# Kernel tuning notes

Hardware: AMD Instinct MI355X
Metric: run time of the kernel (lower is better)

Reference implementation:

```python
import jax, jax.numpy as jnp
import numpy as np

N, KLEN, Q, S, E, H = 8, 512, 16, 128, 256, 8


def setup_inputs() -> dict:
    key = jax.random.key(0)
    ks = jax.random.split(key, 9)
    values = jax.random.normal(ks[0], (N, KLEN, E), dtype=jnp.float32)
    keys = jax.random.normal(ks[1], (N, KLEN, E), dtype=jnp.float32)
    query = jax.random.normal(ks[2], (N, Q, S, E), dtype=jnp.float32)
    mask = jax.random.randint(ks[3], (N, 1, 1, KLEN, 1), 0, 2, dtype=jnp.int32)
    Wv = jax.random.normal(ks[4], (E, E), dtype=jnp.float32) * 0.02
    Wk = jax.random.normal(ks[5], (E, E), dtype=jnp.float32) * 0.02
    Wq = jax.random.normal(ks[6], (E, E), dtype=jnp.float32) * 0.02
    Wo = jax.random.normal(ks[7], (E, H * E), dtype=jnp.float32) * 0.02
    bo = jnp.zeros((E,), dtype=jnp.float32)
    return {"values": values, "keys": keys, "query": query, "mask": mask,
            "Wv": Wv, "Wk": Wk, "Wq": Wq, "Wo": Wo, "bo": bo}


def reference(values, keys, query, mask, Wv, Wk, Wq, Wo, bo):
    # In the torch module head_dim == embed_size and the SAME Linear is applied
    # to every (expanded) head, so project once and broadcast over heads.
    e = Wq.shape[0]
    heads = Wo.shape[1] // e
    v = values @ Wv.T          # [N, K, E]
    k = keys @ Wk.T            # [N, K, E]
    q = query @ Wq.T           # [N, Q, S, E]
    # energy per head is identical; broadcast to [N, H, Q, K, S] to mirror
    # torch's einsum('nqshd,nkhd->nhqks') followed by masked_fill.
    energy = jnp.einsum('nqsd,nkd->nqks', q, k)               # [N, Q, K, S]
    energy = jnp.broadcast_to(energy[:, None],
                              (energy.shape[0], heads) + energy.shape[1:])
    energy = jnp.where(mask == 0, jnp.float32(-1e20), energy)  # [N,H,Q,K,S]
    attn = jax.nn.softmax(energy / jnp.sqrt(jnp.float32(e)), axis=3)
    out = jnp.einsum('nhqks,nkd->nqshd', attn, v)              # [N,Q,S,H,E]
    out = out.reshape(out.shape[0], out.shape[1], out.shape[2], heads * e)
    return out @ Wo.T + bo                                     # [N, Q, S, E]
```

## Files before the change

### kernel.cpp

```cpp
#include <hip/hip_runtime.h>
#include <hip/hip_bf16.h>
#include <stdint.h>

#define NB   8
#define KL   512
#define QD   16
#define SD   128
#define ED   256
#define RPN  (QD*SD)
#define BMR  32
#define FRAG 512
#define PAN  131072

typedef __hip_bfloat16 bf16;
using s16x8 = __attribute__((ext_vector_type(8))) short;
using f32x4 = __attribute__((ext_vector_type(4))) float;

__device__ __forceinline__ float b2f(unsigned short u){
    union { uint32_t i; float f; } v; v.i = ((uint32_t)u) << 16; return v.f;
}
__device__ __forceinline__ float b2f_hi(uint32_t u){
    union { uint32_t i; float f; } v; v.i = u & 0xFFFF0000u; return v.f;
}
__device__ __forceinline__ float b2f_lo(uint32_t u){
    union { uint32_t i; float f; } v; v.i = u << 16; return v.f;
}
__device__ __forceinline__ unsigned short f2b(float f){
    union { float ff; uint32_t i; } v; v.ff = f;
    uint32_t lsb = (v.i >> 16) & 1;
    v.i += 0x7FFFu + lsb;
    return (unsigned short)(v.i >> 16);
}
__device__ __forceinline__ uint32_t cvtpk(float lo, float hi){
    uint32_t r;
    asm("v_cvt_pk_bf16_f32 %0, %1, %2" : "=v"(r) : "v"(lo), "v"(hi));
    return r;
}
__device__ __forceinline__ f32x4 mfma16(s16x8 a, s16x8 b, f32x4 c){
    return __builtin_amdgcn_mfma_f32_16x16x32_bf16(a, b, c, 0, 0, 0);
}

template<bool B>
__device__ __forceinline__ float ldin(const void* p, size_t i){
    if (B) return b2f(((const unsigned short*)p)[i]);
    else   return ((const float*)p)[i];
}

__device__ bool probe_bf16(const uint32_t* __restrict__ w, int* pc){
    if (threadIdx.x == 0) *pc = 0;
    __syncthreads();
    if (threadIdx.x < 256){
        int local = 0;
        #pragma unroll
        for (int i = 0; i < 4; ++i){
            uint32_t x = w[threadIdx.x*4 + i];
            uint32_t e = (x >> 7) & 0xFFu;
            local += (e >= 120u && e <= 132u) ? 1 : 0;
        }
        if (local) atomicAdd(pc, local);
    }
    __syncthreads();
    return *pc > 512;
}

__device__ __forceinline__ int waddr(int i, int o){
    return (((o >> 4)*8 + (i >> 5)) << 9) + (((o & 15) | (((i >> 3) & 3) << 4)) << 3) + (i & 7);
}

template<bool B>
__device__ void gt_body(const void* __restrict__ Wq, const void* __restrict__ Wk,
                        unsigned short* __restrict__ WgH,
                        unsigned short* __restrict__ WgL, int bx){
    int b = bx, a = threadIdx.x;
    float s = 0.f;
    #pragma unroll 8
    for (int d = 0; d < 256; ++d)
        s += ldin<B>(Wq, (size_t)d*256 + a) * ldin<B>(Wk, (size_t)d*256 + b);
    unsigned short hi = f2b(s);
    unsigned short lo = f2b(s - b2f(hi));
    int ad = waddr(b, a);
    WgH[ad] = hi; WgL[ad] = lo;
}
template<bool B>
__device__ void wosmt_body(const void* __restrict__ Wo, const void* __restrict__ Wv,
                           unsigned short* __restrict__ WmH,
                           unsigned short* __restrict__ WmL, int bx, float (*sm)[256]){
    int t = threadIdx.x, e0 = bx*8;
    #pragma unroll
    for (int je = 0; je < 8; ++je){
        int e = e0 + je;
        float s = 0.f;
        #pragma unroll
        for (int h = 0; h < 8; ++h) s += ldin<B>(Wo, (size_t)e*2048 + h*256 + t);
        sm[je][t] = s;
    }
    __syncthreads();
    float acc[8] = {0,0,0,0,0,0,0,0};
    #pragma unroll 4
    for (int dp = 0; dp < 256; ++dp){
        float wv = ldin<B>(Wv, (size_t)dp*256 + t);
        #pragma unroll
        for (int je = 0; je < 8; ++je) acc[je] += sm[je][dp] * wv;
    }
    #pragma unroll
    for (int je = 0; je < 8; ++je){
        unsigned short hi = f2b(acc[je]);
        unsigned short lo = f2b(acc[je] - b2f(hi));
        int ad = waddr(t, e0 + je);
        WmH[ad] = hi; WmL[ad] = lo;
    }
}
__global__ __launch_bounds__(256)
void k_prep(const void* __restrict__ values,
            const void* __restrict__ Wq, const void* __restrict__ Wk,
            const void* __restrict__ Wo, const void* __restrict__ Wv,
            unsigned short* __restrict__ WgH, unsigned short* __restrict__ WgL,
            unsigned short* __restrict__ WmH, unsigned short* __restrict__ WmL){
    __shared__ float sm[8][256];
    __shared__ int pc;
    bool bf = probe_bf16((const uint32_t*)values, &pc);
    if (blockIdx.x < 256){
        if (bf) gt_body<true >(Wq, Wk, WgH, WgL, blockIdx.x);
        else    gt_body<false>(Wq, Wk, WgH, WgL, blockIdx.x);
    } else {
        int bx = blockIdx.x - 256;
        if (bf) wosmt_body<true >(Wo, Wv, WmH, WmL, bx, sm);
        else    wosmt_body<false>(Wo, Wv, WmH, WmL, bx, sm);
    }
}

template<bool B>
__device__ void projM_body(const void* __restrict__ A,
                           const unsigned short* __restrict__ WH,
                           const unsigned short* __restrict__ WL,
                           unsigned short* __restrict__ outF,
                           int bx8, bool keysHalf, unsigned short* St){
    int t = threadIdx.x, lane = t & 63, w = t >> 6;
    int l15 = t & 15, g = (t >> 4) & 3;
    int r0 = bx8 * 16;

    f32x4 acc[2];
    acc[0] = (f32x4){0.f,0.f,0.f,0.f};
    acc[1] = (f32x4){0.f,0.f,0.f,0.f};

    s16x8 wh[3][2], wl[3][2];
    auto LDW = [&](int ks, int sl){
        #pragma unroll
        for (int c = 0; c < 2; ++c){
            size_t off = (size_t)(((w*2 + c)*8 + ks)*512 + lane*8);
            wh[sl][c] = *(const s16x8*)(WH + off);
            wl[sl][c] = *(const s16x8*)(WL + off);
        }
    };
    float4 ar[2][2];
    s16x8  ab[2];
    auto LDA = [&](int ks, int sl){
        size_t idx = (size_t)(r0 + l15)*256 + ks*32 + g*8;
        if (B) ab[sl] = *(const s16x8*)((const unsigned short*)A + idx);
        else { ar[sl][0] = *(const float4*)((const float*)A + idx);
               ar[sl][1] = *(const float4*)((const float*)A + idx + 4); }
    };
    LDW(0,0); LDW(1,1); LDA(0,0); LDA(1,1);

    #pragma unroll
    for (int ks = 0; ks < 8; ++ks){
        int s = ks & 1, sw = ks % 3;
        s16x8 ah, al;
        if (B){
            ah = ab[s];
        } else {
            union { s16x8 v; uint32_t u[4]; } H, L;
            float4 x0 = ar[s][0], x1 = ar[s][1];
            H.u[0] = cvtpk(x0.x, x0.y); H.u[1] = cvtpk(x0.z, x0.w);
            H.u[2] = cvtpk(x1.x, x1.y); H.u[3] = cvtpk(x1.z, x1.w);
            L.u[0] = cvtpk(x0.x - b2f_lo(H.u[0]), x0.y - b2f_hi(H.u[0]));
            L.u[1] = cvtpk(x0.z - b2f_lo(H.u[1]), x0.w - b2f_hi(H.u[1]));
            L.u[2] = cvtpk(x1.x - b2f_lo(H.u[2]), x1.y - b2f_hi(H.u[2]));
            L.u[3] = cvtpk(x1.z - b2f_lo(H.u[3]), x1.w - b2f_hi(H.u[3]));
            ah = H.v; al = L.v;
        }
        if (ks + 2 < 8) LDA(ks + 2, s);
        #pragma unroll
        for (int c = 0; c < 2; ++c){
            acc[c] = mfma16(ah, wh[sw][c], acc[c]);
            if (!B) acc[c] = mfma16(al, wh[sw][c], acc[c]);
            acc[c] = mfma16(ah, wl[sw][c], acc[c]);
        }
        if (ks + 2 < 8) LDW(ks + 2, (ks + 2) % 3);
    }

    int n   = bx8 >> 5;
    int r0n = r0 & 511;
    #pragma unroll
    for (int c = 0; c < 2; ++c){
        #pragma unroll
        for (int j = 0; j < 4; ++j){
            int row = g*4 + j;
            int col = (w*2 + c)*16 + l15;
            int idx;
            if (keysHalf)
                idx = ((col >> 5) << 9) + (((row & 15) | (((col >> 3) & 3) << 4)) << 3) + (col & 7);
            else {
                int key = r0n + row;
                idx = ((col >> 4) << 8) + ((((col & 15) | (((key >> 3) & 1) << 4))) << 3) + (key & 7);
            }
            St[idx] = f2b(acc[c][j]);
        }
    }
    __syncthreads();

    int s8 = t * 8;
    if (keysHalf){
        size_t base = (size_t)n*PAN + (size_t)((r0n >> 4) * 8) * 512;
        *(s16x8*)(outF + base + s8) = *(const s16x8*)(St + s8);
    } else {
        int ks2 = r0n >> 5;
        int fl = s8 >> 8, off = s8 & 255;
        int halfbase = ((r0n >> 4) & 1) * 256;
        *(s16x8*)(outF + (size_t)n*PAN + (size_t)((fl*16 + ks2)*512 + halfbase + off))
            = *(const s16x8*)(St + s8);
    }
}
__global__ __launch_bounds__(512)
void k_projM(const void* __restrict__ keys, const void* __restrict__ values,
             const unsigned short* __restrict__ WgH, const unsigned short* __restrict__ WgL,
             const unsigned short* __restrict__ WmH, const unsigned short* __restrict__ WmL,
             unsigned short* __restrict__ kkF, unsigned short* __restrict__ utF){
    __shared__ unsigned short St[4096];
    __shared__ int pc;
    bool bf = probe_bf16((const uint32_t*)values, &pc);
    int bx = blockIdx.x;
    bool keysHalf = (bx < 256);
    int bx8 = bx & 255;
    if (keysHalf){
        if (bf) projM_body<true >(keys, WgH, WgL, kkF, bx8, true, St);
        else    projM_body<false>(keys, WgH, WgL, kkF, bx8, true, St);
    } else {
        if (bf) projM_body<true >(values, WmH, WmL, utF, bx8, false, St);
        else    projM_body<false>(values, WmH, WmL, utF, bx8, false, St);
    }
}

template<bool B>
__device__ void fused_body(const void* __restrict__ query,
                           const unsigned short* __restrict__ kkF,
                           const unsigned short* __restrict__ utF,
                           const int* __restrict__ mask,
                           const void* __restrict__ bo,
                           void* __restrict__ out,
                           unsigned short* Qs, unsigned short* Pf,
                           float* redM, float* redS){
    int bid = blockIdx.x;
    int n   = bid & 7;
    int r0  = (bid >> 3) * BMR;
    int t   = threadIdx.x;
    int l15 = t & 15;
    int g   = (t >> 4) & 3;
    int w   = t >> 6;
    int lane = t & 63;

    const unsigned short* Kn = kkF + (size_t)n*PAN;
    const unsigned short* Un = utF + (size_t)n*PAN;
    const int* mn = mask + n*KL;

    {
        int row = t >> 4;
        int c0  = (t & 15) * 16;
        int sw  = (row & 7) << 3;
        size_t qoff = (size_t)n*RPN*ED + (size_t)(r0 + row)*ED + c0;
        if (B){
            const unsigned short* qp = (const unsigned short*)query + qoff;
            s16x8 v0 = *(const s16x8*)(qp);
            s16x8 v1 = *(const s16x8*)(qp + 8);
            *(s16x8*)&Qs[(row*ED + c0    ) ^ sw] = v0;
            *(s16x8*)&Qs[(row*ED + c0 + 8) ^ sw] = v1;
        } else {
            const float* qp = (const float*)query + qoff;
            float4 x0 = *(const float4*)(qp);
            float4 x1 = *(const float4*)(qp + 4);
            float4 x2 = *(const float4*)(qp + 8);
            float4 x3 = *(const float4*)(qp + 12);
            union { s16x8 v; uint32_t u[4]; } pk;
            pk.u[0] = cvtpk(x0.x,x0.y); pk.u[1] = cvtpk(x0.z,x0.w);
            pk.u[2] = cvtpk(x1.x,x1.y); pk.u[3] = cvtpk(x1.z,x1.w);
            *(s16x8*)&Qs[(row*ED + c0    ) ^ sw] = pk.v;
            pk.u[0] = cvtpk(x2.x,x2.y); pk.u[1] = cvtpk(x2.z,x2.w);
            pk.u[2] = cvtpk(x3.x,x3.y); pk.u[3] = cvtpk(x3.z,x3.w);
            *(s16x8*)&Qs[(row*ED + c0 + 8) ^ sw] = pk.v;
        }
    }
    __syncthreads();

    int asw = (l15 & 7) << 3;

    float p[2][4][4];
    {
        f32x4 acc1[2][4];
        #pragma unroll
        for (int rt = 0; rt < 2; ++rt)
            #pragma unroll
            for (int c = 0; c < 4; ++c) acc1[rt][c] = (f32x4){0.f,0.f,0.f,0.f};

        const unsigned short* kb = Kn + (size_t)w*16384 + (size_t)lane*8;
        s16x8 bb[3][4];
        auto LDK = [&](int KS, int SL){
            #pragma unroll
            for (int c = 0; c < 4; ++c)
                bb[SL][c] = *(const s16x8*)(kb + (size_t)(c*8 + KS)*FRAG);
        };
        LDK(0,0); LDK(1,1);
        #pragma unroll
        for (int ks = 0; ks < 8; ++ks){
            if (ks + 2 < 8) LDK(ks + 2, (ks + 2) % 3);
            int col = ks*32 + g*8;
            s16x8 a0 = *(const s16x8*)&Qs[(( 0 + l15)*ED + col) ^ asw];
            s16x8 a1 = *(const s16x8*)&Qs[((16 + l15)*ED + col) ^ asw];
            #pragma unroll
            for (int c = 0; c < 4; ++c){
                acc1[0][c] = mfma16(a0, bb[ks % 3][c], acc1[0][c]);
                acc1[1][c] = mfma16(a1, bb[ks % 3][c], acc1[1][c]);
            }
        }
        #pragma unroll
        for (int c = 0; c < 4; ++c){
            bool zz = (mn[w*64 + c*16 + l15] == 0);
            #pragma unroll
            for (int rt = 0; rt < 2; ++rt)
                #pragma unroll
                for (int j = 0; j < 4; ++j)
                    p[rt][c][j] = zz ? -1e20f : acc1[rt][c][j] * 0.0625f;
        }
    }

    {
        float mx[2][4];
        #pragma unroll
        for (int rt = 0; rt < 2; ++rt)
            #pragma unroll
            for (int j = 0; j < 4; ++j){
                float m0 = fmaxf(fmaxf(p[rt][0][j], p[rt][1][j]),
                                 fmaxf(p[rt][2][j], p[rt][3][j]));
                #pragma unroll
                for (int off = 1; off < 16; off <<= 1)
                    m0 = fmaxf(m0, __shfl_xor(m0, off, 16));
                mx[rt][j] = m0;
            }
        if (l15 == 0){
            #pragma unroll
            for (int rt = 0; rt < 2; ++rt)
                #pragma unroll
                for (int j = 0; j < 4; ++j)
                    redM[(rt*16 + g*4 + j)*8 + w] = mx[rt][j];
        }
        __syncthreads();
        float sm[2][4];
        #pragma unroll
        for (int rt = 0; rt < 2; ++rt)
            #pragma unroll
            for (int j = 0; j < 4; ++j){
                int row = rt*16 + g*4 + j;
                float4 a = *(const float4*)&redM[row*8];
                float4 b = *(const float4*)&redM[row*8 + 4];
                float m = fmaxf(fmaxf(fmaxf(a.x,a.y),fmaxf(a.z,a.w)),
                                fmaxf(fmaxf(b.x,b.y),fmaxf(b.z,b.w)));
                float s = 0.f;
                #pragma unroll
                for (int c = 0; c < 4; ++c){
                    p[rt][c][j] = __expf(p[rt][c][j] - m);
                    s += p[rt][c][j];
                }
                #pragma unroll
                for (int off = 1; off < 16; off <<= 1)
                    s += __shfl_xor(s, off, 16);
                sm[rt][j] = s;
            }
        if (l15 == 0){
            #pragma unroll
            for (int rt = 0; rt < 2; ++rt)
                #pragma unroll
                for (int j = 0; j < 4; ++j)
                    redS[(rt*16 + g*4 + j)*8 + w] = sm[rt][j];
        }
        __syncthreads();
        int ihi = ((l15 >> 3) << 4);
        int ilo = l15 & 7;
        #pragma unroll
        for (int rt = 0; rt < 2; ++rt){
            #pragma unroll
            for (int j = 0; j < 4; ++j){
                int row = rt*16 + g*4 + j;
                float4 a = *(const float4*)&redS[row*8];
                float4 b = *(const float4*)&redS[row*8 + 4];
                float inv = 1.0f / ((a.x+a.y+a.z+a.w) + (b.x+b.y+b.z+b.w));
                #pragma unroll
                for (int c = 0; c < 4; ++c){
                    int lp = (g*4 + j) | (((c & 1) << 5) | ihi);
                    int elem = (rt*16 + w*2 + (c >> 1))*FRAG + lp*8 + ilo;
                    Pf[elem] = f2b(p[rt][c][j] * inv);
                }
            }
        }
    }
    __syncthreads();

    {
        f32x4 acc2[2][2];
        #pragma unroll
        for (int rt = 0; rt < 2; ++rt)
            #pragma unroll
            for (int c = 0; c < 2; ++c) acc2[rt][c] = (f32x4){0.f,0.f,0.f,0.f};

        const unsigned short* ub = Un + (size_t)(2*w)*8192 + (size_t)lane*8;
        s16x8 bu[3][2];
        auto LDU = [&](int KS, int SL){
            #pragma unroll
            for (int c = 0; c < 2; ++c)
                bu[SL][c] = *(const s16x8*)(ub + (size_t)(c*16 + KS)*FRAG);
        };
        LDU(0,0); LDU(1,1);
        #pragma unroll
        for (int ks = 0; ks < 16; ++ks){
            if (ks + 2 < 16) LDU(ks + 2, (ks + 2) % 3);
            s16x8 p0 = *(const s16x8*)&Pf[( 0 + ks)*FRAG + lane*8];
            s16x8 p1 = *(const s16x8*)&Pf[(16 + ks)*FRAG + lane*8];
            #pragma unroll
            for (int c = 0; c < 2; ++c){
                acc2[0][c] = mfma16(p0, bu[ks % 3][c], acc2[0][c]);
                acc2[1][c] = mfma16(p1, bu[ks % 3][c], acc2[1][c]);
            }
        }
        float bov[2];
        #pragma unroll
        for (int c = 0; c < 2; ++c) bov[c] = ldin<B>(bo, (2*w + c)*16 + l15);
        #pragma unroll
        for (int rt = 0; rt < 2; ++rt){
            #pragma unroll
            for (int j = 0; j < 4; ++j){
                int row = rt*16 + g*4 + j;
                #pragma unroll
                for (int c = 0; c < 2; ++c){
                    int e = (2*w + c)*16 + l15;
                    float val = acc2[rt][c][j] + bov[c];
                    size_t oidx = (size_t)n*RPN*ED + (size_t)(r0 + row)*ED + e;
                    if (B) ((unsigned short*)out)[oidx] = f2b(val);
                    else   ((float*)out)[oidx] = val;
                }
            }
        }
    }
}

__global__ __launch_bounds__(512, 4)
void k_fused4(const void* __restrict__ values, const void* __restrict__ query,
              const unsigned short* __restrict__ kkF,
              const unsigned short* __restrict__ utF,
              const int* __restrict__ mask, const void* __restrict__ bo,
              void* __restrict__ out){
    __shared__ unsigned short Qs[BMR*ED];
    __shared__ unsigned short Pf[32*FRAG];
    __shared__ float redM[BMR*8];
    __shared__ float redS[BMR*8];
    __shared__ int pc;
    bool bf = probe_bf16((const uint32_t*)values, &pc);
    if (bf) fused_body<true >(query, kkF, utF, mask, bo, out, Qs, Pf, redM, redS);
    else    fused_body<false>(query, kkF, utF, mask, bo, out, Qs, Pf, redM, redS);
}

extern "C" void kernel_launch(void* const* d_in, const int* in_sizes, int n_in,
                              void* d_out, int out_size, void* d_ws, size_t ws_size,
                              hipStream_t stream){
    const void* values = d_in[0];
    const void* keys   = d_in[1];
    const void* query  = d_in[2];
    const int*  mask   = (const int*)d_in[3];
    const void* Wv     = d_in[4];
    const void* Wk     = d_in[5];
    const void* Wq     = d_in[6];
    const void* Wo     = d_in[7];
    const void* bo     = d_in[8];

    unsigned short* wsu = (unsigned short*)d_ws;
    unsigned short* wgh = wsu;
    unsigned short* wgl = wsu + 65536;
    unsigned short* wmh = wsu + 131072;
    unsigned short* wml = wsu + 196608;
    unsigned short* ws_kk = wsu + 262144;
    unsigned short* ws_u  = ws_kk + (size_t)NB*PAN;

    k_prep  <<< 288, 256, 0, stream>>>(values, Wq, Wk, Wo, Wv, wgh, wgl, wmh, wml);
    k_projM <<< 512, 512, 0, stream>>>(keys, values, wgh, wgl, wmh, wml, ws_kk, ws_u);
    k_fused4<<< 512, 512, 0, stream>>>(values, query, ws_kk, ws_u, mask, bo, d_out);
}
```

Measured before the change: 142.7 us.

## Double row tiles per block in projection and fused attention kernels

Both the projection kernel and the fused attention kernel now handle twice as many rows per block (32 rows in projection, 64 query rows in fused), so each block reuses every loaded weight, K and U fragment across more MFMA tiles. The grids shrink from 512 to 256 blocks, the shared staging and P buffers double, and the fused kernel's launch bound drops to 2 blocks per CU. This cuts redundant global loads of K/V panels and weights, but raises register and LDS pressure and leaves fewer blocks to fill the 256 CUs.

```diff
diff --git a/kernel.cpp b/kernel.cpp
--- a/kernel.cpp
+++ b/kernel.cpp
@@ -8,7 +8,7 @@
 #define SD   128
 #define ED   256
 #define RPN  (QD*SD)
-#define BMR  32
+#define BMR  64
 #define FRAG 512
 #define PAN  131072
 
@@ -134,14 +134,18 @@
                            const unsigned short* __restrict__ WH,
                            const unsigned short* __restrict__ WL,
                            unsigned short* __restrict__ outF,
-                           int bx8, bool keysHalf, unsigned short* St){
+                           int bx, bool keysHalf, unsigned short* St){
     int t = threadIdx.x, lane = t & 63, w = t >> 6;
     int l15 = t & 15, g = (t >> 4) & 3;
-    int r0 = bx8 * 16;
-
-    f32x4 acc[2];
-    acc[0] = (f32x4){0.f,0.f,0.f,0.f};
-    acc[1] = (f32x4){0.f,0.f,0.f,0.f};
+    int n   = bx >> 4;
+    int r0n = (bx & 15) * 32;
+    int r0  = n*512 + r0n;
+
+    f32x4 acc[2][2];
+    #pragma unroll
+    for (int rt = 0; rt < 2; ++rt)
+        #pragma unroll
+        for (int c = 0; c < 2; ++c) acc[rt][c] = (f32x4){0.f,0.f,0.f,0.f};
 
     s16x8 wh[3][2], wl[3][2];
     auto LDW = [&](int ks, int sl){
@@ -152,73 +156,86 @@
             wl[sl][c] = *(const s16x8*)(WL + off);
         }
     };
-    float4 ar[2][2];
-    s16x8  ab[2];
+    float4 ar[2][2][2];
+    s16x8  ab[2][2];
     auto LDA = [&](int ks, int sl){
-        size_t idx = (size_t)(r0 + l15)*256 + ks*32 + g*8;
-        if (B) ab[sl] = *(const s16x8*)((const unsigned short*)A + idx);
-        else { ar[sl][0] = *(const float4*)((const float*)A + idx);
-               ar[sl][1] = *(const float4*)((const float*)A + idx + 4); }
+        #pragma unroll
+        for (int rt = 0; rt < 2; ++rt){
+            size_t idx = (size_t)(r0 + rt*16 + l15)*256 + ks*32 + g*8;
+            if (B) ab[sl][rt] = *(const s16x8*)((const unsigned short*)A + idx);
+            else { ar[sl][rt][0] = *(const float4*)((const float*)A + idx);
+                   ar[sl][rt][1] = *(const float4*)((const float*)A + idx + 4); }
+        }
     };
     LDW(0,0); LDW(1,1); LDA(0,0); LDA(1,1);
 
     #pragma unroll
     for (int ks = 0; ks < 8; ++ks){
         int s = ks & 1, sw = ks % 3;
-        s16x8 ah, al;
-        if (B){
-            ah = ab[s];
+        s16x8 ah[2], al[2];
+        #pragma unroll
+        for (int rt = 0; rt < 2; ++rt){
+            if (B){
+                ah[rt] = ab[s][rt];
+            } else {
+                union { s16x8 v; uint32_t u[4]; } H, L;
+                float4 x0 = ar[s][rt][0], x1 = ar[s][rt][1];
+                H.u[0] = cvtpk(x0.x, x0.y); H.u[1] = cvtpk(x0.z, x0.w);
+                H.u[2] = cvtpk(x1.x, x1.y); H.u[3] = cvtpk(x1.z, x1.w);
+                L.u[0] = cvtpk(x0.x - b2f_lo(H.u[0]), x0.y - b2f_hi(H.u[0]));
+                L.u[1] = cvtpk(x0.z - b2f_lo(H.u[1]), x0.w - b2f_hi(H.u[1]));
+                L.u[2] = cvtpk(x1.x - b2f_lo(H.u[2]), x1.y - b2f_hi(H.u[2]));
+                L.u[3] = cvtpk(x1.z - b2f_lo(H.u[3]), x1.w - b2f_hi(H.u[3]));
+                ah[rt] = H.v; al[rt] = L.v;
+            }
+        }
+        if (ks + 2 < 8) LDA(ks + 2, s);
+        #pragma unroll
+        for (int rt = 0; rt < 2; ++rt)
+            #pragma unroll
+            for (int c = 0; c < 2; ++c){
+                acc[rt][c] = mfma16(ah[rt], wh[sw][c], acc[rt][c]);
+                if (!B) acc[rt][c] = mfma16(al[rt], wh[sw][c], acc[rt][c]);
+                acc[rt][c] = mfma16(ah[rt], wl[sw][c], acc[rt][c]);
+            }
+        if (ks + 2 < 8) LDW(ks + 2, (ks + 2) % 3);
+    }
+
+    #pragma unroll
+    for (int rt = 0; rt < 2; ++rt){
+        #pragma unroll
+        for (int c = 0; c < 2; ++c){
+            #pragma unroll
+            for (int j = 0; j < 4; ++j){
+                int rloc = g*4 + j;
+                int col  = (w*2 + c)*16 + l15;
+                int idx;
+                if (keysHalf)
+                    idx = rt*4096 + ((col >> 5) << 9)
+                        + ((rloc | (((col >> 3) & 3) << 4)) << 3) + (col & 7);
+                else {
+                    int kl = rt*16 + rloc;
+                    idx = ((col >> 4) << 9)
+                        + (((col & 15) | ((kl >> 3) << 4)) << 3) + (kl & 7);
+                }
+                St[idx] = f2b(acc[rt][c][j]);
+            }
+        }
+    }
+    __syncthreads();
+
+    #pragma unroll
+    for (int h = 0; h < 2; ++h){
+        int s8 = t*8 + h*4096;
+        if (keysHalf){
+            size_t base = (size_t)n*PAN + (size_t)((r0n >> 4)*8)*512;
+            *(s16x8*)(outF + base + s8) = *(const s16x8*)(St + s8);
         } else {
-            union { s16x8 v; uint32_t u[4]; } H, L;
-            float4 x0 = ar[s][0], x1 = ar[s][1];
-            H.u[0] = cvtpk(x0.x, x0.y); H.u[1] = cvtpk(x0.z, x0.w);
-            H.u[2] = cvtpk(x1.x, x1.y); H.u[3] = cvtpk(x1.z, x1.w);
-            L.u[0] = cvtpk(x0.x - b2f_lo(H.u[0]), x0.y - b2f_hi(H.u[0]));
-            L.u[1] = cvtpk(x0.z - b2f_lo(H.u[1]), x0.w - b2f_hi(H.u[1]));
-            L.u[2] = cvtpk(x1.x - b2f_lo(H.u[2]), x1.y - b2f_hi(H.u[2]));
-            L.u[3] = cvtpk(x1.z - b2f_lo(H.u[3]), x1.w - b2f_hi(H.u[3]));
-            ah = H.v; al = L.v;
-        }
-        if (ks + 2 < 8) LDA(ks + 2, s);
-        #pragma unroll
-        for (int c = 0; c < 2; ++c){
-            acc[c] = mfma16(ah, wh[sw][c], acc[c]);
-            if (!B) acc[c] = mfma16(al, wh[sw][c], acc[c]);
-            acc[c] = mfma16(ah, wl[sw][c], acc[c]);
-        }
-        if (ks + 2 < 8) LDW(ks + 2, (ks + 2) % 3);
-    }
-
-    int n   = bx8 >> 5;
-    int r0n = r0 & 511;
-    #pragma unroll
-    for (int c = 0; c < 2; ++c){
-        #pragma unroll
-        for (int j = 0; j < 4; ++j){
-            int row = g*4 + j;
-            int col = (w*2 + c)*16 + l15;
-            int idx;
-            if (keysHalf)
-                idx = ((col >> 5) << 9) + (((row & 15) | (((col >> 3) & 3) << 4)) << 3) + (col & 7);
-            else {
-                int key = r0n + row;
-                idx = ((col >> 4) << 8) + ((((col & 15) | (((key >> 3) & 1) << 4))) << 3) + (key & 7);
-            }
-            St[idx] = f2b(acc[c][j]);
-        }
-    }
-    __syncthreads();
-
-    int s8 = t * 8;
-    if (keysHalf){
-        size_t base = (size_t)n*PAN + (size_t)((r0n >> 4) * 8) * 512;
-        *(s16x8*)(outF + base + s8) = *(const s16x8*)(St + s8);
-    } else {
-        int ks2 = r0n >> 5;
-        int fl = s8 >> 8, off = s8 & 255;
-        int halfbase = ((r0n >> 4) & 1) * 256;
-        *(s16x8*)(outF + (size_t)n*PAN + (size_t)((fl*16 + ks2)*512 + halfbase + off))
-            = *(const s16x8*)(St + s8);
+            int ks2 = r0n >> 5;
+            int fl = s8 >> 9, off = s8 & 511;
+            *(s16x8*)(outF + (size_t)n*PAN + (size_t)((fl*16 + ks2)*512 + off))
+                = *(const s16x8*)(St + s8);
+        }
     }
 }
 __global__ __launch_bounds__(512)
@@ -226,18 +243,18 @@
              const unsigned short* __restrict__ WgH, const unsigned short* __restrict__ WgL,
              const unsigned short* __restrict__ WmH, const unsigned short* __restrict__ WmL,
              unsigned short* __restrict__ kkF, unsigned short* __restrict__ utF){
-    __shared__ unsigned short St[4096];
+    __shared__ unsigned short St[8192];
     __shared__ int pc;
     bool bf = probe_bf16((const uint32_t*)values, &pc);
     int bx = blockIdx.x;
-    bool keysHalf = (bx < 256);
-    int bx8 = bx & 255;
+    bool keysHalf = (bx < 128);
+    int bxl = bx & 127;
     if (keysHalf){
-        if (bf) projM_body<true >(keys, WgH, WgL, kkF, bx8, true, St);
-        else    projM_body<false>(keys, WgH, WgL, kkF, bx8, true, St);
+        if (bf) projM_body<true >(keys, WgH, WgL, kkF, bxl, true, St);
+        else    projM_body<false>(keys, WgH, WgL, kkF, bxl, true, St);
     } else {
-        if (bf) projM_body<true >(values, WmH, WmL, utF, bx8, false, St);
-        else    projM_body<false>(values, WmH, WmL, utF, bx8, false, St);
+        if (bf) projM_body<true >(values, WmH, WmL, utF, bxl, false, St);
+        else    projM_body<false>(values, WmH, WmL, utF, bxl, false, St);
     }
 }
 
@@ -263,8 +280,9 @@
     const unsigned short* Un = utF + (size_t)n*PAN;
     const int* mn = mask + n*KL;
 
-    {
-        int row = t >> 4;
+    #pragma unroll
+    for (int rr = 0; rr < 2; ++rr){
+        int row = rr*32 + (t >> 4);
         int c0  = (t & 15) * 16;
         int sw  = (row & 7) << 3;
         size_t qoff = (size_t)n*RPN*ED + (size_t)(r0 + row)*ED + c0;
@@ -293,11 +311,10 @@
 
     int asw = (l15 & 7) << 3;
 
-    float p[2][4][4];
+    f32x4 acc1[4][4];
     {
-        f32x4 acc1[2][4];
-        #pragma unroll
-        for (int rt = 0; rt < 2; ++rt)
+        #pragma unroll
+        for (int rt = 0; rt < 4; ++rt)
             #pragma unroll
             for (int c = 0; c < 4; ++c) acc1[rt][c] = (f32x4){0.f,0.f,0.f,0.f};
 
@@ -313,49 +330,40 @@
         for (int ks = 0; ks < 8; ++ks){
             if (ks + 2 < 8) LDK(ks + 2, (ks + 2) % 3);
             int col = ks*32 + g*8;
-            s16x8 a0 = *(const s16x8*)&Qs[(( 0 + l15)*ED + col) ^ asw];
-            s16x8 a1 = *(const s16x8*)&Qs[((16 + l15)*ED + col) ^ asw];
-            #pragma unroll
-            for (int c = 0; c < 4; ++c){
-                acc1[0][c] = mfma16(a0, bb[ks % 3][c], acc1[0][c]);
-                acc1[1][c] = mfma16(a1, bb[ks % 3][c], acc1[1][c]);
+            #pragma unroll
+            for (int rt = 0; rt < 4; ++rt){
+                s16x8 a = *(const s16x8*)&Qs[((rt*16 + l15)*ED + col) ^ asw];
+                #pragma unroll
+                for (int c = 0; c < 4; ++c)
+                    acc1[rt][c] = mfma16(a, bb[ks % 3][c], acc1[rt][c]);
             }
         }
         #pragma unroll
         for (int c = 0; c < 4; ++c){
             bool zz = (mn[w*64 + c*16 + l15] == 0);
             #pragma unroll
-            for (int rt = 0; rt < 2; ++rt)
+            for (int rt = 0; rt < 4; ++rt)
                 #pragma unroll
                 for (int j = 0; j < 4; ++j)
-                    p[rt][c][j] = zz ? -1e20f : acc1[rt][c][j] * 0.0625f;
+                    acc1[rt][c][j] = zz ? -1e20f : acc1[rt][c][j] * 0.0625f;
         }
     }
 
     {
-        float mx[2][4];
-        #pragma unroll
-        for (int rt = 0; rt < 2; ++rt)
+        #pragma unroll
+        for (int rt = 0; rt < 4; ++rt)
             #pragma unroll
             for (int j = 0; j < 4; ++j){
-                float m0 = fmaxf(fmaxf(p[rt][0][j], p[rt][1][j]),
-                                 fmaxf(p[rt][2][j], p[rt][3][j]));
+                float m0 = fmaxf(fmaxf(acc1[rt][0][j], acc1[rt][1][j]),
+                                 fmaxf(acc1[rt][2][j], acc1[rt][3][j]));
                 #pragma unroll
                 for (int off = 1; off < 16; off <<= 1)
                     m0 = fmaxf(m0, __shfl_xor(m0, off, 16));
-                mx[rt][j] = m0;
-            }
-        if (l15 == 0){
-            #pragma unroll
-            for (int rt = 0; rt < 2; ++rt)
-                #pragma unroll
-                for (int j = 0; j < 4; ++j)
-                    redM[(rt*16 + g*4 + j)*8 + w] = mx[rt][j];
-        }
+                if (l15 == 0) redM[(rt*16 + g*4 + j)*8 + w] = m0;
+            }
         __syncthreads();
-        float sm[2][4];
-        #pragma unroll
-        for (int rt = 0; rt < 2; ++rt)
+        #pragma unroll
+        for (int rt = 0; rt < 4; ++rt)
             #pragma unroll
             for (int j = 0; j < 4; ++j){
                 int row = rt*16 + g*4 + j;
@@ -366,26 +374,19 @@
                 float s = 0.f;
                 #pragma unroll
                 for (int c = 0; c < 4; ++c){
-                    p[rt][c][j] = __expf(p[rt][c][j] - m);
-                    s += p[rt][c][j];
+                    acc1[rt][c][j] = __expf(acc1[rt][c][j] - m);
+                    s += acc1[rt][c][j];
                 }
                 #pragma unroll
                 for (int off = 1; off < 16; off <<= 1)
                     s += __shfl_xor(s, off, 16);
-                sm[rt][j] = s;
-            }
-        if (l15 == 0){
-            #pragma unroll
-            for (int rt = 0; rt < 2; ++rt)
-                #pragma unroll
-                for (int j = 0; j < 4; ++j)
-                    redS[(rt*16 + g*4 + j)*8 + w] = sm[rt][j];
-        }
+                if (l15 == 0) redS[row*8 + w] = s;
+            }
         __syncthreads();
         int ihi = ((l15 >> 3) << 4);
         int ilo = l15 & 7;
         #pragma unroll
-        for (int rt = 0; rt < 2; ++rt){
+        for (int rt = 0; rt < 4; ++rt){
             #pragma unroll
             for (int j = 0; j < 4; ++j){
                 int row = rt*16 + g*4 + j;
@@ -396,7 +397,7 @@
                 for (int c = 0; c < 4; ++c){
                     int lp = (g*4 + j) | (((c & 1) << 5) | ihi);
                     int elem = (rt*16 + w*2 + (c >> 1))*FRAG + lp*8 + ilo;
-                    Pf[elem] = f2b(p[rt][c][j] * inv);
+                    Pf[elem] = f2b(acc1[rt][c][j] * inv);
                 }
             }
         }
@@ -404,9 +405,9 @@
     __syncthreads();
 
     {
-        f32x4 acc2[2][2];
-        #pragma unroll
-        for (int rt = 0; rt < 2; ++rt)
+        f32x4 acc2[4][2];
+        #pragma unroll
+        for (int rt = 0; rt < 4; ++rt)
             #pragma unroll
             for (int c = 0; c < 2; ++c) acc2[rt][c] = (f32x4){0.f,0.f,0.f,0.f};
 
@@ -421,19 +422,19 @@
         #pragma unroll
         for (int ks = 0; ks < 16; ++ks){
             if (ks + 2 < 16) LDU(ks + 2, (ks + 2) % 3);
-            s16x8 p0 = *(const s16x8*)&Pf[( 0 + ks)*FRAG + lane*8];
-            s16x8 p1 = *(const s16x8*)&Pf[(16 + ks)*FRAG + lane*8];
-            #pragma unroll
-            for (int c = 0; c < 2; ++c){
-                acc2[0][c] = mfma16(p0, bu[ks % 3][c], acc2[0][c]);
-                acc2[1][c] = mfma16(p1, bu[ks % 3][c], acc2[1][c]);
+            #pragma unroll
+            for (int rt = 0; rt < 4; ++rt){
+                s16x8 p = *(const s16x8*)&Pf[(rt*16 + ks)*FRAG + lane*8];
+                #pragma unroll
+                for (int c = 0; c < 2; ++c)
+                    acc2[rt][c] = mfma16(p, bu[ks % 3][c], acc2[rt][c]);
             }
         }
         float bov[2];
         #pragma unroll
         for (int c = 0; c < 2; ++c) bov[c] = ldin<B>(bo, (2*w + c)*16 + l15);
         #pragma unroll
-        for (int rt = 0; rt < 2; ++rt){
+        for (int rt = 0; rt < 4; ++rt){
             #pragma unroll
             for (int j = 0; j < 4; ++j){
                 int row = rt*16 + g*4 + j;
@@ -450,14 +451,14 @@
     }
 }
 
-__global__ __launch_bounds__(512, 4)
-void k_fused4(const void* __restrict__ values, const void* __restrict__ query,
+__global__ __launch_bounds__(512, 2)
+void k_fused5(const void* __restrict__ values, const void* __restrict__ query,
               const unsigned short* __restrict__ kkF,
               const unsigned short* __restrict__ utF,
               const int* __restrict__ mask, const void* __restrict__ bo,
               void* __restrict__ out){
     __shared__ unsigned short Qs[BMR*ED];
-    __shared__ unsigned short Pf[32*FRAG];
+    __shared__ unsigned short Pf[64*FRAG];
     __shared__ float redM[BMR*8];
     __shared__ float redS[BMR*8];
     __shared__ int pc;
@@ -488,6 +489,6 @@
     unsigned short* ws_u  = ws_kk + (size_t)NB*PAN;
 
     k_prep  <<< 288, 256, 0, stream>>>(values, Wq, Wk, Wo, Wv, wgh, wgl, wmh, wml);
-    k_projM <<< 512, 512, 0, stream>>>(keys, values, wgh, wgl, wmh, wml, ws_kk, ws_u);
-    k_fused4<<< 512, 512, 0, stream>>>(values, query, ws_kk, ws_u, mask, bo, d_out);
-}
+    k_projM <<< 256, 512, 0, stream>>>(keys, values, wgh, wgl, wmh, wml, ws_kk, ws_u);
+    k_fused5<<< 256, 512, 0, stream>>>(values, query, ws_kk, ws_u, mask, bo, d_out);
+}
```

Measured after the change: 144.8 us. Within noise of the previous version (+1.5%).
